# Kernel optimization log

Hardware: AMD Instinct MI355X
Metric: run time of the kernel (lower is better)

The kernel has to match this reference:

```python
import jax, jax.numpy as jnp
import numpy as np

EMBED_DIM = 1024
NUM_HEADS = 16
HEAD_DIM = EMBED_DIM // NUM_HEADS


def setup_inputs() -> dict:
    key = jax.random.key(0)
    k_x, k_qkv, k_ow, k_ob = jax.random.split(key, 4)
    B, N, D = 4, 2048, EMBED_DIM
    x = jax.random.normal(k_x, (B, N, D), dtype=jnp.float32)
    # nn.Linear(D, 3D, bias=False): weight [3D, D], y = x @ W.T
    w_qkv = jax.random.normal(k_qkv, (3 * D, D), dtype=jnp.float32) * (D ** -0.5)
    # nn.Linear(D, D): weight [D, D], bias [D]
    w_out = jax.random.normal(k_ow, (D, D), dtype=jnp.float32) * (D ** -0.5)
    b_out = jax.random.normal(k_ob, (D,), dtype=jnp.float32) * 0.01
    return {"x": x, "w_qkv": w_qkv, "w_out": w_out, "b_out": b_out}


def reference(x, w_qkv, w_out, b_out):
    B, N, D = x.shape
    H, Hd = NUM_HEADS, HEAD_DIM
    scale = Hd ** -0.5
    qkv = x @ w_qkv.T                              # [B, N, 3D]
    q, k, v = jnp.split(qkv, 3, axis=-1)
    q = q.reshape(B, N, H, Hd).transpose(0, 2, 1, 3)  # [B, H, N, Hd]
    k = k.reshape(B, N, H, Hd).transpose(0, 2, 1, 3)
    v = v.reshape(B, N, H, Hd).transpose(0, 2, 1, 3)
    scores = jnp.einsum('bhnd,bhmd->bhnm', q, k) * scale  # [B, H, N, N]
    attn = jax.nn.softmax(scores, axis=-1)
    out = jnp.einsum('bhnm,bhmd->bhnd', attn, v)   # [B, H, N, Hd]
    out = out.transpose(0, 2, 1, 3).reshape(B, N, D)
    return out @ w_out.T + b_out
```

## Files before the change

### kernel.cpp

```cpp
#include <hip/hip_runtime.h>
#include <math.h>

#define SEQ   2048
#define BATCH 4
#define NH    16
#define HD    64
#define DDIM  1024

typedef __attribute__((ext_vector_type(8))) short short8;
typedef __attribute__((ext_vector_type(4))) float f32x4;

#define QSCALE 0.18033688011112042f
#define C2     14.426950408889634f

__device__ __forceinline__ ushort f2bf(float f) {
  union { float f; unsigned u; } x; x.f = f;
  unsigned r = x.u + 0x7fffu + ((x.u >> 16) & 1u);
  return (ushort)(r >> 16);
}

#if __has_builtin(__builtin_amdgcn_cvt_pk_bf16_f32)
typedef __attribute__((ext_vector_type(2))) __bf16 bf16x2;
__device__ __forceinline__ unsigned pk2bf(float a, float b) {
  union { bf16x2 v; unsigned u; } x;
  x.v = __builtin_amdgcn_cvt_pk_bf16_f32(a, b);
  return x.u;
}
#else
__device__ __forceinline__ unsigned pk2bf(float a, float b) {
  return (unsigned)f2bf(a) | ((unsigned)f2bf(b) << 16);
}
#endif

__device__ __forceinline__ void gll16(const ushort* g, ushort* l) {
  __builtin_amdgcn_global_load_lds(
      (const __attribute__((address_space(1))) unsigned int*)g,
      (__attribute__((address_space(3))) unsigned int*)l, 16, 0, 0);
}

__global__ __launch_bounds__(256) void conv_bf16(
    const float* __restrict__ in, ushort* __restrict__ out) {
  size_t i = ((size_t)blockIdx.x * 256 + threadIdx.x) * 4;
  float4 v = *(const float4*)(in + i);
  uint2 u;
  u.x = pk2bf(v.x, v.y);
  u.y = pk2bf(v.z, v.w);
  *(uint2*)(out + i) = u;
}

__device__ __forceinline__ void gemm_nt_core(
    const ushort* __restrict__ A, const ushort* __restrict__ B,
    ushort* As, ushort* Bs, f32x4 (&acc)[4][4], int m0, int n0) {
  const int tid = threadIdx.x;
  const int lane = tid & 63;
  const int w = tid >> 6;
  const int KD = 1024;

  const int rA = lane >> 2;
  const int gg = (lane & 3) ^ ((lane >> 3) & 3);
  const ushort* ag0 = A + (size_t)(m0 + w * 32 + rA) * KD + gg * 8;
  const ushort* ag1 = ag0 + (size_t)16 * KD;
  const ushort* bg0 = B + (size_t)(n0 + w * 32 + rA) * KD + gg * 8;
  const ushort* bg1 = bg0 + (size_t)16 * KD;
  ushort* al0 = As + (w * 32) * 32;  ushort* al1 = al0 + 16 * 32;
  ushort* bl0 = Bs + (w * 32) * 32;  ushort* bl1 = bl0 + 16 * 32;

  const int fr = lane & 15;
  const int fg = lane >> 4;
  const int fo = (fg ^ ((fr >> 1) & 3)) * 8;
  const int wm = (w & 1) * 64, wn = (w >> 1) * 64;

  for (int kt = 0; kt < KD; kt += 32) {
    __syncthreads();
    gll16(ag0 + kt, al0);
    gll16(ag1 + kt, al1);
    gll16(bg0 + kt, bl0);
    gll16(bg1 + kt, bl1);
    __syncthreads();
    short8 af[4], bf[4];
#pragma unroll
    for (int t = 0; t < 4; ++t) {
      af[t] = *(const short8*)&As[(wm + t * 16 + fr) * 32 + fo];
      bf[t] = *(const short8*)&Bs[(wn + t * 16 + fr) * 32 + fo];
    }
#pragma unroll
    for (int mt = 0; mt < 4; ++mt)
#pragma unroll
      for (int nt = 0; nt < 4; ++nt)
        acc[mt][nt] = __builtin_amdgcn_mfma_f32_16x16x32_bf16(
            af[mt], bf[nt], acc[mt][nt], 0, 0, 0);
  }
}

__global__ __launch_bounds__(256) void gemm_qkv(
    const ushort* __restrict__ A, const ushort* __restrict__ B,
    ushort* __restrict__ Qb, ushort* __restrict__ Kb, ushort* __restrict__ Vtb) {
  __shared__ ushort smem[9216];
  ushort* As = smem;
  ushort* Bs = smem + 4096;
  const int m0 = blockIdx.y * 128, n0 = blockIdx.x * 128;
  f32x4 acc[4][4] = {};
  gemm_nt_core(A, B, As, Bs, acc, m0, n0);

  const int lane = threadIdx.x & 63;
  const int w = threadIdx.x >> 6;
  const int wm = (w & 1) * 64, wn = (w >> 1) * 64;
  const int cr = (lane >> 4) * 4;
  const int cc = lane & 15;

  if (n0 >= 2048) {
    ushort* T = smem;
    const int b = m0 >> 11;
    const int rbase = m0 & 2047;
    const int tid = threadIdx.x;
#pragma unroll
    for (int p = 0; p < 2; ++p) {
      __syncthreads();
      if ((w >> 1) == p) {
#pragma unroll
        for (int mt = 0; mt < 4; ++mt)
#pragma unroll
          for (int nt = 0; nt < 4; ++nt) {
            const int nl = nt * 16 + cc;
            const int ml = wm + mt * 16 + cr;
#pragma unroll
            for (int jp = 0; jp < 2; ++jp) {
              unsigned u = pk2bf(acc[mt][nt][2 * jp], acc[mt][nt][2 * jp + 1]);
              *(unsigned*)&T[nl * 138 + ml + 2 * jp] = u;
            }
          }
      }
      __syncthreads();
      const int nl = tid >> 2, c0 = (tid & 3) * 32;
      const int d = (n0 - 2048) + p * 64 + nl;
      const int h = d >> 6, dd = d & 63;
      ushort* gdst = Vtb + ((size_t)(b * 16 + h) * 64 + dd) * 2048 + rbase + c0;
#pragma unroll
      for (int q = 0; q < 4; ++q)
        *(short8*)(gdst + q * 8) = *(const short8*)&T[nl * 138 + c0 + q * 8];
    }
  } else {
    const float qs = (n0 < 1024) ? QSCALE : 1.0f;
    ushort* dst = (n0 < 1024) ? Qb : Kb;
    const int nb = (n0 < 1024) ? n0 : n0 - 1024;
#pragma unroll
    for (int mt = 0; mt < 4; ++mt) {
#pragma unroll
      for (int nt = 0; nt < 4; ++nt) {
        const int n = nb + wn + nt * 16 + cc;
        const int h = n >> 6, d = n & 63;
#pragma unroll
        for (int j = 0; j < 4; ++j) {
          const int m = m0 + wm + mt * 16 + cr + j;
          const int b = m >> 11, r = m & 2047;
          dst[(((size_t)(b * 16 + h) * 2048 + r) << 6) + d] =
              f2bf(acc[mt][nt][j] * qs);
        }
      }
    }
  }
}

__global__ __launch_bounds__(256) void gemm_out(
    const ushort* __restrict__ A, const ushort* __restrict__ B,
    const float* __restrict__ bias, float* __restrict__ C) {
  __shared__ ushort smem[8192];
  ushort* As = smem;
  ushort* Bs = smem + 4096;
  const int m0 = blockIdx.y * 128, n0 = blockIdx.x * 128;
  f32x4 acc[4][4] = {};
  gemm_nt_core(A, B, As, Bs, acc, m0, n0);

  const int lane = threadIdx.x & 63;
  const int w = threadIdx.x >> 6;
  const int wm = (w & 1) * 64, wn = (w >> 1) * 64;
  const int cr = (lane >> 4) * 4;
  const int cc = lane & 15;
#pragma unroll
  for (int mt = 0; mt < 4; ++mt) {
#pragma unroll
    for (int nt = 0; nt < 4; ++nt) {
      const int n = n0 + wn + nt * 16 + cc;
      const float bj = bias[n];
#pragma unroll
      for (int j = 0; j < 4; ++j) {
        const int m = m0 + wm + mt * 16 + cr + j;
        C[(size_t)m * 1024 + n] = acc[mt][nt][j] + bj;
      }
    }
  }
}

__global__ __launch_bounds__(256) void attn_bf16(
    const ushort* __restrict__ Qb, const ushort* __restrict__ Kb,
    const ushort* __restrict__ Vtb, ushort* __restrict__ attn) {
  const int b = blockIdx.z, h = blockIdx.y, q0 = blockIdx.x * 64;
  const int tid = threadIdx.x, lane = tid & 63, w = tid >> 6;

  __shared__ ushort Qs[64 * 64];
  __shared__ ushort Ks[64 * 64];
  __shared__ ushort Vts[64 * 64];
  __shared__ ushort Ps[64 * 64];

  const size_t head = (size_t)(b * 16 + h) * (2048 * 64);

  {
    const int r = tid >> 2, cb = (tid & 3) * 2;
    const ushort* qp = Qb + head + (size_t)(q0 + r) * 64 + cb * 8;
    short8 a = *(const short8*)qp;
    short8 bv = *(const short8*)(qp + 8);
    const int sw = r & 7;
    *(short8*)&Qs[r * 64 + ((cb ^ sw) * 8)] = a;
    *(short8*)&Qs[r * 64 + (((cb + 1) ^ sw) * 8)] = bv;
  }

  const int rk = lane >> 3;
  const int ggk = (lane & 7) ^ rk;
  const ushort* kg0 = Kb + head + (size_t)(w * 16 + rk) * 64 + ggk * 8;
  const ushort* kg1 = kg0 + 8 * 64;
  const ushort* vg0 = Vtb + head + (size_t)(w * 16 + rk) * 2048 + ggk * 8;
  const ushort* vg1 = vg0 + 8 * 2048;
  ushort* kl0 = Ks + (w * 16) * 64;   ushort* kl1 = kl0 + 8 * 64;
  ushort* vl0 = Vts + (w * 16) * 64;  ushort* vl1 = vl0 + 8 * 64;

  const int fr = lane & 15;
  const int fg = lane >> 4;
  const int fr7 = fr & 7;

  f32x4 oacc[4] = {};
  float rs[4] = {0.f, 0.f, 0.f, 0.f};

  for (int kt = 0; kt < SEQ / 64; ++kt) {
    __syncthreads();
    gll16(kg0 + kt * 4096, kl0);
    gll16(kg1 + kt * 4096, kl1);
    gll16(vg0 + kt * 64, vl0);
    gll16(vg1 + kt * 64, vl1);
    __syncthreads();

    f32x4 sacc[4] = {{-C2, -C2, -C2, -C2}, {-C2, -C2, -C2, -C2},
                     {-C2, -C2, -C2, -C2}, {-C2, -C2, -C2, -C2}};
#pragma unroll
    for (int ks = 0; ks < 2; ++ks) {
      short8 aq = *(const short8*)&Qs[(w * 16 + fr) * 64 + (((ks * 4 + fg) ^ fr7) * 8)];
#pragma unroll
      for (int nt = 0; nt < 4; ++nt) {
        short8 bk = *(const short8*)
            &Ks[(nt * 16 + fr) * 64 + (((ks * 4 + fg) ^ fr7) * 8)];
        sacc[nt] = __builtin_amdgcn_mfma_f32_16x16x32_bf16(aq, bk, sacc[nt], 0, 0, 0);
      }
    }

#pragma unroll
    for (int nt = 0; nt < 4; ++nt) {
      const int colb = nt * 2 + (fr >> 3);
#pragma unroll
      for (int j = 0; j < 4; j += 2) {
        const float p0 = exp2f(sacc[nt][j]);
        const float p1 = exp2f(sacc[nt][j + 1]);
        rs[j] += p0;
        rs[j + 1] += p1;
        const unsigned pk = pk2bf(p0, p1);
        const int r0 = w * 16 + fg * 4 + j;
        const int r1 = r0 + 1;
        Ps[r0 * 64 + ((colb ^ (r0 & 7)) * 8) + fr7] = (ushort)pk;
        Ps[r1 * 64 + ((colb ^ (r1 & 7)) * 8) + fr7] = (ushort)(pk >> 16);
      }
    }

#pragma unroll
    for (int ks = 0; ks < 2; ++ks) {
      short8 ap = *(const short8*)&Ps[(w * 16 + fr) * 64 + (((ks * 4 + fg) ^ fr7) * 8)];
#pragma unroll
      for (int nt = 0; nt < 4; ++nt) {
        short8 bv = *(const short8*)
            &Vts[(nt * 16 + fr) * 64 + (((ks * 4 + fg) ^ fr7) * 8)];
        oacc[nt] = __builtin_amdgcn_mfma_f32_16x16x32_bf16(ap, bv, oacc[nt], 0, 0, 0);
      }
    }
  }

#pragma unroll
  for (int j = 0; j < 4; ++j) {
#pragma unroll
    for (int mask = 1; mask < 16; mask <<= 1)
      rs[j] += __shfl_xor(rs[j], mask);
    const float inv = 1.f / rs[j];
    const int row = q0 + w * 16 + fg * 4 + j;
#pragma unroll
    for (int nt = 0; nt < 4; ++nt) {
      attn[(size_t)(b * SEQ + row) * DDIM + h * 64 + nt * 16 + fr] =
          f2bf(oacc[nt][j] * inv);
    }
  }
}

extern "C" void kernel_launch(void* const* d_in, const int* in_sizes, int n_in,
                              void* d_out, int out_size, void* d_ws, size_t ws_size,
                              hipStream_t stream) {
  const float* x     = (const float*)d_in[0];
  const float* w_qkv = (const float*)d_in[1];
  const float* w_out = (const float*)d_in[2];
  const float* b_out = (const float*)d_in[3];
  float* out = (float*)d_out;

  ushort* Ax    = (ushort*)d_ws;
  ushort* Wq    = Ax + (size_t)8192 * 1024;
  ushort* Wo    = Wq + (size_t)3072 * 1024;
  ushort* Qb    = Wo + (size_t)1024 * 1024;
  ushort* Kb    = Qb + (size_t)BATCH * NH * SEQ * HD;
  ushort* Vtb   = Kb + (size_t)BATCH * NH * SEQ * HD;
  ushort* attnb = Vtb + (size_t)BATCH * NH * SEQ * HD;

  conv_bf16<<<8192, 256, 0, stream>>>(x, Ax);
  conv_bf16<<<3072, 256, 0, stream>>>(w_qkv, Wq);
  conv_bf16<<<1024, 256, 0, stream>>>(w_out, Wo);

  gemm_qkv<<<dim3(3072 / 128, 8192 / 128), 256, 0, stream>>>(Ax, Wq, Qb, Kb, Vtb);
  attn_bf16<<<dim3(SEQ / 64, NH, BATCH), 256, 0, stream>>>(Qb, Kb, Vtb, attnb);
  gemm_out<<<dim3(1024 / 128, 8192 / 128), 256, 0, stream>>>(attnb, Wo, b_out, out);
}
```

Before: 340.8 us.

## Double-buffer K/V tiles and keep softmax probabilities in registers

The attention kernel now double-buffers the K and V^T shared-memory tiles. The next tile's async loads are issued before computing on the current one, which removes one barrier per iteration. It also swaps the MFMA operands for QK^T, so the score accumulator is transposed and the exponentiated probabilities can be packed directly into the A-operand layout of the PV MFMA. That drops the Ps shared-memory round trip. Row sums become a single per-lane scalar, reduced across lane groups and redistributed with shuffles, and V fragments are loaded as two 4-element halves to match the new k ordering.

```diff
diff --git a/kernel.cpp b/kernel.cpp
--- a/kernel.cpp
+++ b/kernel.cpp
@@ -8,6 +8,7 @@
 #define DDIM  1024
 
 typedef __attribute__((ext_vector_type(8))) short short8;
+typedef __attribute__((ext_vector_type(4))) short short4v;
 typedef __attribute__((ext_vector_type(4))) float f32x4;
 
 #define QSCALE 0.18033688011112042f
@@ -198,9 +199,8 @@
   const int tid = threadIdx.x, lane = tid & 63, w = tid >> 6;
 
   __shared__ ushort Qs[64 * 64];
-  __shared__ ushort Ks[64 * 64];
-  __shared__ ushort Vts[64 * 64];
-  __shared__ ushort Ps[64 * 64];
+  __shared__ ushort Ks[2][64 * 64];
+  __shared__ ushort Vts[2][64 * 64];
 
   const size_t head = (size_t)(b * 16 + h) * (2048 * 64);
 
@@ -220,23 +220,33 @@
   const ushort* kg1 = kg0 + 8 * 64;
   const ushort* vg0 = Vtb + head + (size_t)(w * 16 + rk) * 2048 + ggk * 8;
   const ushort* vg1 = vg0 + 8 * 2048;
-  ushort* kl0 = Ks + (w * 16) * 64;   ushort* kl1 = kl0 + 8 * 64;
-  ushort* vl0 = Vts + (w * 16) * 64;  ushort* vl1 = vl0 + 8 * 64;
+  ushort* klb[2] = {&Ks[0][(w * 16) * 64], &Ks[1][(w * 16) * 64]};
+  ushort* vlb[2] = {&Vts[0][(w * 16) * 64], &Vts[1][(w * 16) * 64]};
 
   const int fr = lane & 15;
   const int fg = lane >> 4;
   const int fr7 = fr & 7;
 
   f32x4 oacc[4] = {};
-  float rs[4] = {0.f, 0.f, 0.f, 0.f};
+  float rs = 0.f;
+
+  gll16(kg0, klb[0]);
+  gll16(kg1, klb[0] + 8 * 64);
+  gll16(vg0, vlb[0]);
+  gll16(vg1, vlb[0] + 8 * 64);
 
   for (int kt = 0; kt < SEQ / 64; ++kt) {
     __syncthreads();
-    gll16(kg0 + kt * 4096, kl0);
-    gll16(kg1 + kt * 4096, kl1);
-    gll16(vg0 + kt * 64, vl0);
-    gll16(vg1 + kt * 64, vl1);
-    __syncthreads();
+    const int cur = kt & 1;
+    if (kt + 1 < SEQ / 64) {
+      const int nxt = cur ^ 1;
+      gll16(kg0 + (kt + 1) * 4096, klb[nxt]);
+      gll16(kg1 + (kt + 1) * 4096, klb[nxt] + 8 * 64);
+      gll16(vg0 + (kt + 1) * 64, vlb[nxt]);
+      gll16(vg1 + (kt + 1) * 64, vlb[nxt] + 8 * 64);
+    }
+    const ushort* K = &Ks[cur][0];
+    const ushort* V = &Vts[cur][0];
 
     f32x4 sacc[4] = {{-C2, -C2, -C2, -C2}, {-C2, -C2, -C2, -C2},
                      {-C2, -C2, -C2, -C2}, {-C2, -C2, -C2, -C2}};
@@ -246,51 +256,60 @@
 #pragma unroll
       for (int nt = 0; nt < 4; ++nt) {
         short8 bk = *(const short8*)
-            &Ks[(nt * 16 + fr) * 64 + (((ks * 4 + fg) ^ fr7) * 8)];
-        sacc[nt] = __builtin_amdgcn_mfma_f32_16x16x32_bf16(aq, bk, sacc[nt], 0, 0, 0);
-      }
-    }
-
-#pragma unroll
-    for (int nt = 0; nt < 4; ++nt) {
-      const int colb = nt * 2 + (fr >> 3);
-#pragma unroll
-      for (int j = 0; j < 4; j += 2) {
-        const float p0 = exp2f(sacc[nt][j]);
-        const float p1 = exp2f(sacc[nt][j + 1]);
-        rs[j] += p0;
-        rs[j + 1] += p1;
-        const unsigned pk = pk2bf(p0, p1);
-        const int r0 = w * 16 + fg * 4 + j;
-        const int r1 = r0 + 1;
-        Ps[r0 * 64 + ((colb ^ (r0 & 7)) * 8) + fr7] = (ushort)pk;
-        Ps[r1 * 64 + ((colb ^ (r1 & 7)) * 8) + fr7] = (ushort)(pk >> 16);
-      }
-    }
-
+            &K[(nt * 16 + fr) * 64 + (((ks * 4 + fg) ^ fr7) * 8)];
+        sacc[nt] = __builtin_amdgcn_mfma_f32_16x16x32_bf16(bk, aq, sacc[nt], 0, 0, 0);
+      }
+    }
+
+    short8 pa[2];
 #pragma unroll
     for (int ks = 0; ks < 2; ++ks) {
-      short8 ap = *(const short8*)&Ps[(w * 16 + fr) * 64 + (((ks * 4 + fg) ^ fr7) * 8)];
+      const float e0 = exp2f(sacc[2 * ks][0]);
+      const float e1 = exp2f(sacc[2 * ks][1]);
+      const float e2 = exp2f(sacc[2 * ks][2]);
+      const float e3 = exp2f(sacc[2 * ks][3]);
+      const float e4 = exp2f(sacc[2 * ks + 1][0]);
+      const float e5 = exp2f(sacc[2 * ks + 1][1]);
+      const float e6 = exp2f(sacc[2 * ks + 1][2]);
+      const float e7 = exp2f(sacc[2 * ks + 1][3]);
+      rs += ((e0 + e1) + (e2 + e3)) + ((e4 + e5) + (e6 + e7));
+      union { unsigned u[4]; short8 s8; } P;
+      P.u[0] = pk2bf(e0, e1);
+      P.u[1] = pk2bf(e2, e3);
+      P.u[2] = pk2bf(e4, e5);
+      P.u[3] = pk2bf(e6, e7);
+      pa[ks] = P.s8;
+    }
+
+#pragma unroll
+    for (int ks = 0; ks < 2; ++ks) {
+      const int e0 = ks * 32 + fg * 4;
+      const int e1 = e0 + 16;
+      const int o0 = ((e0 >> 3) ^ fr7) * 8 + (e0 & 7);
+      const int o1 = ((e1 >> 3) ^ fr7) * 8 + (e1 & 7);
 #pragma unroll
       for (int nt = 0; nt < 4; ++nt) {
-        short8 bv = *(const short8*)
-            &Vts[(nt * 16 + fr) * 64 + (((ks * 4 + fg) ^ fr7) * 8)];
-        oacc[nt] = __builtin_amdgcn_mfma_f32_16x16x32_bf16(ap, bv, oacc[nt], 0, 0, 0);
-      }
-    }
-  }
+        const int row = (nt * 16 + fr) * 64;
+        union { short4v h[2]; short8 s8; } Bf;
+        Bf.h[0] = *(const short4v*)&V[row + o0];
+        Bf.h[1] = *(const short4v*)&V[row + o1];
+        oacc[nt] = __builtin_amdgcn_mfma_f32_16x16x32_bf16(pa[ks], Bf.s8, oacc[nt], 0, 0, 0);
+      }
+    }
+  }
+
+  rs += __shfl_xor(rs, 16);
+  rs += __shfl_xor(rs, 32);
+  const float inv = 1.f / rs;
 
 #pragma unroll
   for (int j = 0; j < 4; ++j) {
-#pragma unroll
-    for (int mask = 1; mask < 16; mask <<= 1)
-      rs[j] += __shfl_xor(rs[j], mask);
-    const float inv = 1.f / rs[j];
+    const float invj = __shfl(inv, fg * 4 + j);
     const int row = q0 + w * 16 + fg * 4 + j;
 #pragma unroll
     for (int nt = 0; nt < 4; ++nt) {
       attn[(size_t)(b * SEQ + row) * DDIM + h * 64 + nt * 16 + fr] =
-          f2bf(oacc[nt][j] * inv);
+          f2bf(oacc[nt][j] * invj);
     }
   }
 }
```

After: 354.5 us. 1.04x slower.
